# Optimization experiments

Hardware: AMD Instinct MI355X
Metric: run time of the kernel (lower is better)

## Reference

```python
import jax, jax.numpy as jnp
import numpy as np

B, N, E, D = 4, 4096, 2048, 128
MAX_L = 10


def setup_inputs() -> dict:
    key = jax.random.key(0)
    ks = jax.random.split(key, 8)
    x = jax.random.normal(ks[0], (B, N, D), dtype=jnp.float32)
    incidence = jax.random.uniform(ks[1], (B, N, E), dtype=jnp.float32)
    edge_orders = jax.random.randint(ks[2], (B, E), 0, MAX_L + 1)
    # positive normalizer to avoid division blow-up
    prefix_normalizer = jax.random.uniform(ks[3], (B, E), dtype=jnp.float32) + 0.5
    node_mask = jnp.ones((B, N), dtype=bool)
    edge_mask = jnp.ones((B, E), dtype=bool)
    n_nodes = jnp.full((B,), float(N), dtype=jnp.float32)
    # learned tables: Positional2DWeight(2, max_l+1, D, D) and PositionalWeight(max_l+1, 1, D)
    w_table = jax.random.normal(ks[4], (2, MAX_L + 1, D, D), dtype=jnp.float32) * (1.0 / np.sqrt(D))
    b_table = jax.random.normal(ks[5], (MAX_L + 1, D), dtype=jnp.float32) * 0.02
    return {"x": x, "incidence": incidence, "edge_orders": edge_orders,
            "prefix_normalizer": prefix_normalizer, "node_mask": node_mask,
            "edge_mask": edge_mask, "n_nodes": n_nodes,
            "w_table": w_table, "b_table": b_table}


def reference(x, incidence, edge_orders, prefix_normalizer, node_mask, edge_mask,
              n_nodes, w_table, b_table):
    # mask invalid nodes
    x = jnp.where(node_mask[..., None], x, 0.0)  # [B,N,D]
    # per-edge weight gather (the duplicated [B,E,D,D] tensors)
    w0 = w_table[0][edge_orders]  # [B,E,D,D]
    w1 = w_table[1][edge_orders]  # [B,E,D,D]
    w0_1 = w_table[0, 1]          # [D,D]
    w1_1 = w_table[1, 1]          # [D,D]
    # global mean pooling over nodes
    x0 = jnp.sum(x, axis=1, keepdims=True) / n_nodes[:, None, None]  # [B,1,D]
    # incidence-based V2E aggregation
    x1_e = jnp.einsum('bne,bnd->bed', incidence, x) / prefix_normalizer[..., None]
    x1_e = jnp.where(edge_mask[..., None], x1_e, 0.0)  # [B,E,D]
    # node branch: shared order-1 weights
    x_v = jnp.einsum('bnd,do->bno', x0, w0_1) + jnp.einsum('bnd,do->bno', x, w1_1)
    # edge branch: per-edge-order weights
    x_e = jnp.einsum('bd,bedo->beo', x0[:, 0], w0) + jnp.einsum('bed,bedo->beo', x1_e, w1)
    x_v = jnp.where(node_mask[..., None], x_v, 0.0)
    x_e = jnp.where(edge_mask[..., None], x_e, 0.0)
    # BiasE
    bias_e = b_table[edge_orders]            # [B,E,D]
    bias_1 = b_table[1][None, None, :]       # [1,1,D]
    x_v = jnp.where(node_mask[..., None], x_v + bias_1, 0.0)
    x_e = jnp.where(edge_mask[..., None], x_e + bias_e, 0.0)
    return x_v, x_e
```

## Files before the change

kernel.cpp:

```cpp
#include <hip/hip_runtime.h>

#define Bb 4
#define Nn 4096
#define Ee 2048
#define Dd 128
#define NL 11
#define TE 32
#define NCH 64

typedef unsigned short u16;
typedef unsigned int u32;
typedef __attribute__((ext_vector_type(8))) short short8;
typedef __attribute__((ext_vector_type(4))) float floatx4;

__device__ __forceinline__ u16 f2bf(float f) {
    union { float f; u32 i; } v; v.f = f;
    u32 r = v.i + 0x7fffu + ((v.i >> 16) & 1u);
    return (u16)(r >> 16);
}
__device__ __forceinline__ u32 pack2(float lo, float hi) {
    return (u32)f2bf(lo) | ((u32)f2bf(hi) << 16);
}

__global__ __launch_bounds__(128) void k_pool(const float* __restrict__ x,
                                              float* __restrict__ ws) {
    int b = blockIdx.x, ch = blockIdx.y, d = threadIdx.x;
    const float* p = x + ((size_t)b * Nn + (size_t)ch * 64) * Dd + d;
    float s = 0.f;
    for (int i = 0; i < 64; i++) s += p[(size_t)i * Dd];
    atomicAdd(&ws[b * Dd + d], s);
}

__global__ __launch_bounds__(128) void k_xe0(const float* __restrict__ ws,
                                             const float* __restrict__ wt,
                                             float* __restrict__ xe0) {
    int b = blockIdx.x, l = blockIdx.y, o = threadIdx.x;
    const float* w0 = wt + (size_t)l * Dd * Dd + o;
    float acc = 0.f;
    for (int d = 0; d < Dd; ++d)
        acc += ws[b * Dd + d] * w0[(size_t)d * Dd];
    xe0[(b * NL + l) * Dd + o] = acc * (1.0f / Nn);
}

__global__ __launch_bounds__(256) void k_trx(const float* __restrict__ x,
                                             u32* __restrict__ xt) {
    int b = blockIdx.x, n0 = blockIdx.y * 32, d0 = blockIdx.z * 32;
    int t = threadIdx.x;
    __shared__ float tile[32][33];
    int r = t >> 5, c = t & 31;
#pragma unroll
    for (int i = 0; i < 4; i++)
        tile[r + 8 * i][c] = x[((size_t)b * Nn + n0 + r + 8 * i) * Dd + d0 + c];
    __syncthreads();
#pragma unroll
    for (int i = 0; i < 2; i++) {
        int idx = t + 256 * i;
        int dl = idx >> 4, cp = idx & 15;
        u32 v = pack2(tile[2 * cp][dl], tile[2 * cp + 1][dl]);
        xt[(size_t)(b * Dd + d0 + dl) * (Nn / 2) + (n0 >> 1) + cp] = v;
    }
}

__global__ __launch_bounds__(256) void k_xv(const float* __restrict__ x,
                                            const float* __restrict__ wt,
                                            const float* __restrict__ bt,
                                            const float* __restrict__ xe0,
                                            float* __restrict__ outv) {
    int b = blockIdx.x, n0 = blockIdx.y * 32, t = threadIdx.x;
    __shared__ float xls[32][129];
    const float4* xs = (const float4*)(x + ((size_t)b * Nn + n0) * Dd);
#pragma unroll
    for (int i = 0; i < 4; i++) {
        int idx = t + 256 * i;
        int r = idx >> 5, c4 = idx & 31;
        float4 v = xs[idx];
        xls[r][c4 * 4 + 0] = v.x; xls[r][c4 * 4 + 1] = v.y;
        xls[r][c4 * 4 + 2] = v.z; xls[r][c4 * 4 + 3] = v.w;
    }
    __syncthreads();
    int o = t & 127, h = t >> 7;
    float base = xe0[(b * NL + 1) * Dd + o] + bt[Dd + o];
    float acc[16];
#pragma unroll
    for (int r = 0; r < 16; r++) acc[r] = base;
    const float* w11 = wt + (size_t)(NL + 1) * Dd * Dd + o;
    for (int d = 0; d < Dd; d++) {
        float wv = w11[(size_t)d * Dd];
#pragma unroll
        for (int r = 0; r < 16; r++) acc[r] += xls[h * 16 + r][d] * wv;
    }
    float* op = outv + ((size_t)b * Nn + n0 + h * 16) * Dd + o;
#pragma unroll
    for (int r = 0; r < 16; r++) op[(size_t)r * Dd] = acc[r];
}

__global__ __launch_bounds__(512) void k_edge(const float* __restrict__ inc,
                                              const u32* __restrict__ xt,
                                              const int* __restrict__ ord,
                                              const float* __restrict__ pref,
                                              const float* __restrict__ wt,
                                              const float* __restrict__ bt,
                                              const float* __restrict__ xe0,
                                              float* __restrict__ oute) {
    int b = blockIdx.x, et0 = blockIdx.y * TE;
    int t = threadIdx.x;
    __shared__ u32 incT[TE][36];
    __shared__ float x1s[TE][Dd + 1];
    __shared__ int ls[TE];
    __shared__ float pv[TE];
    if (t < TE) {
        ls[t] = ord[b * Ee + et0 + t];
        pv[t] = pref[b * Ee + et0 + t];
    }

    int lane = t & 63, w = t >> 6;
    int lm = lane & 15, quad = lane >> 4;
    int etile = w & 1, dt0 = (w >> 1) * 2;
    int eA = etile * 16 + lm;
    floatx4 acc0 = {0.f, 0.f, 0.f, 0.f}, acc1 = {0.f, 0.f, 0.f, 0.f};

    const u32* bb0 = xt + (size_t)(b * Dd + dt0 * 16 + lm) * (Nn / 2) + quad * 4;
    const u32* bb1 = xt + (size_t)(b * Dd + (dt0 + 1) * 16 + lm) * (Nn / 2) + quad * 4;
    int sn = t >> 3, sc4 = t & 7;

    for (int n0 = 0; n0 < Nn; n0 += NCH) {
        int ko = n0 >> 1;
        short8 b00 = *(const short8*)(bb0 + ko);
        short8 b10 = *(const short8*)(bb1 + ko);
        short8 b01 = *(const short8*)(bb0 + ko + 16);
        short8 b11 = *(const short8*)(bb1 + ko + 16);
        if (t < 256) {
            const float4* ra =
                (const float4*)(inc + ((size_t)b * Nn + n0 + 2 * sn) * Ee + et0);
            float4 va = ra[sc4];
            float4 vb = ra[sc4 + Ee / 4];
            incT[sc4 * 4 + 0][sn] = pack2(va.x, vb.x);
            incT[sc4 * 4 + 1][sn] = pack2(va.y, vb.y);
            incT[sc4 * 4 + 2][sn] = pack2(va.z, vb.z);
            incT[sc4 * 4 + 3][sn] = pack2(va.w, vb.w);
        }
        __syncthreads();
        short8 a0 = *(const short8*)&incT[eA][quad * 4];
        acc0 = __builtin_amdgcn_mfma_f32_16x16x32_bf16(a0, b00, acc0, 0, 0, 0);
        acc1 = __builtin_amdgcn_mfma_f32_16x16x32_bf16(a0, b10, acc1, 0, 0, 0);
        short8 a1 = *(const short8*)&incT[eA][16 + quad * 4];
        acc0 = __builtin_amdgcn_mfma_f32_16x16x32_bf16(a1, b01, acc0, 0, 0, 0);
        acc1 = __builtin_amdgcn_mfma_f32_16x16x32_bf16(a1, b11, acc1, 0, 0, 0);
        __syncthreads();
    }

#pragma unroll
    for (int r = 0; r < 4; r++) {
        int e = etile * 16 + quad * 4 + r;
        float rp = 1.0f / pv[e];
        x1s[e][dt0 * 16 + lm] = acc0[r] * rp;
        x1s[e][(dt0 + 1) * 16 + lm] = acc1[r] * rp;
    }
    __syncthreads();

    int o = t & 127, h = t >> 7;
    const float* w1base = wt + (size_t)NL * Dd * Dd;
    for (int j = 0; j < 8; j++) {
        int e = h * 8 + j;
        int l = ls[e];
        const float* w1 = w1base + (size_t)l * Dd * Dd + o;
        float a = xe0[(b * NL + l) * Dd + o] + bt[l * Dd + o];
#pragma unroll 4
        for (int d = 0; d < Dd; d++) a += x1s[e][d] * w1[(size_t)d * Dd];
        oute[((size_t)b * Ee + et0 + e) * Dd + o] = a;
    }
}

extern "C" void kernel_launch(void* const* d_in, const int* in_sizes, int n_in,
                              void* d_out, int out_size, void* d_ws,
                              size_t ws_size, hipStream_t stream) {
    const float* x    = (const float*)d_in[0];
    const float* inc  = (const float*)d_in[1];
    const int*   ord  = (const int*)d_in[2];
    const float* pref = (const float*)d_in[3];
    const float* wt   = (const float*)d_in[7];
    const float* bt   = (const float*)d_in[8];

    float* outv = (float*)d_out;
    float* oute = outv + (size_t)Bb * Nn * Dd;

    float* ws  = (float*)d_ws;
    float* xe0 = ws + 512;
    u32*   xt  = (u32*)(ws + 8192);

    hipMemsetAsync(d_ws, 0, 512 * sizeof(float), stream);
    k_pool<<<dim3(Bb, 64), 128, 0, stream>>>(x, ws);
    k_xe0<<<dim3(Bb, NL), 128, 0, stream>>>(ws, wt, xe0);
    k_trx<<<dim3(Bb, Nn / 32, Dd / 32), 256, 0, stream>>>(x, xt);
    k_xv<<<dim3(Bb, Nn / 32), 256, 0, stream>>>(x, wt, bt, xe0, outv);
    k_edge<<<dim3(Bb, Ee / TE), 512, 0, stream>>>(inc, xt, ord, pref, wt, bt,
                                                  xe0, oute);
}
```

Baseline: 335.9 us.

## Split edge kernel into pipelined MFMA einsum and order-bucketed MFMA epilogue

The fused edge kernel is replaced by three parts. A double-buffered, register-prefetched bf16 MFMA kernel computes the incidence-x aggregation into a bf16 intermediate. Edges are then bucketed by order with count, prefix and scatter kernels, so a grouped MFMA epilogue can apply each order's weight matrix from LDS. The node branch also moves from scalar FP32 FMAs to bf16 MFMA. This removes the per-edge scalar matvec and the globally re-read weights, at the cost of extra launches, atomics and more bf16 rounding of weights and activations.

```diff
diff --git a/kernel.cpp b/kernel.cpp
--- a/kernel.cpp
+++ b/kernel.cpp
@@ -5,8 +5,6 @@
 #define Ee 2048
 #define Dd 128
 #define NL 11
-#define TE 32
-#define NCH 64
 
 typedef unsigned short u16;
 typedef unsigned int u32;
@@ -19,26 +17,29 @@
     return (u16)(r >> 16);
 }
 __device__ __forceinline__ u32 pack2(float lo, float hi) {
-    return (u32)f2bf(lo) | ((u32)f2bf(hi) << 16);
-}
+    union { float f; u32 i; } a, b; a.f = lo; b.f = hi;
+    u32 x = a.i + 0x7fffu + ((a.i >> 16) & 1u);
+    u32 y = b.i + 0x7fffu + ((b.i >> 16) & 1u);
+    return (x >> 16) | (y & 0xffff0000u);
+}
+union S8U { u32 u[4]; short8 s; };
 
 __global__ __launch_bounds__(128) void k_pool(const float* __restrict__ x,
-                                              float* __restrict__ ws) {
+                                              float* __restrict__ sums) {
     int b = blockIdx.x, ch = blockIdx.y, d = threadIdx.x;
     const float* p = x + ((size_t)b * Nn + (size_t)ch * 64) * Dd + d;
     float s = 0.f;
     for (int i = 0; i < 64; i++) s += p[(size_t)i * Dd];
-    atomicAdd(&ws[b * Dd + d], s);
-}
-
-__global__ __launch_bounds__(128) void k_xe0(const float* __restrict__ ws,
+    atomicAdd(&sums[b * Dd + d], s);
+}
+
+__global__ __launch_bounds__(128) void k_xe0(const float* __restrict__ sums,
                                              const float* __restrict__ wt,
                                              float* __restrict__ xe0) {
     int b = blockIdx.x, l = blockIdx.y, o = threadIdx.x;
     const float* w0 = wt + (size_t)l * Dd * Dd + o;
     float acc = 0.f;
-    for (int d = 0; d < Dd; ++d)
-        acc += ws[b * Dd + d] * w0[(size_t)d * Dd];
+    for (int d = 0; d < Dd; ++d) acc += sums[b * Dd + d] * w0[(size_t)d * Dd];
     xe0[(b * NL + l) * Dd + o] = acc * (1.0f / Nn);
 }
 
@@ -54,10 +55,109 @@
     __syncthreads();
 #pragma unroll
     for (int i = 0; i < 2; i++) {
-        int idx = t + 256 * i;
-        int dl = idx >> 4, cp = idx & 15;
+        int idx2 = t + 256 * i;
+        int dl = idx2 >> 4, cp = idx2 & 15;
         u32 v = pack2(tile[2 * cp][dl], tile[2 * cp + 1][dl]);
         xt[(size_t)(b * Dd + d0 + dl) * (Nn / 2) + (n0 >> 1) + cp] = v;
+    }
+}
+
+__global__ __launch_bounds__(256) void k_count(const int* __restrict__ ord,
+                                               int* __restrict__ cnt) {
+    int gid = blockIdx.x * 256 + threadIdx.x;
+    int b = gid >> 11, e = gid & 2047;
+    atomicAdd(&cnt[b * NL + ord[b * Ee + e]], 1);
+}
+__global__ __launch_bounds__(64) void k_prefix(const int* __restrict__ cnt,
+                                               int* __restrict__ offs,
+                                               int* __restrict__ idx) {
+    int t = threadIdx.x;
+    if (t == 0) {
+        int off = 0;
+        for (int i = 0; i < Bb * NL; i++) {
+            offs[i] = off;
+            off += (cnt[i] + 15) & ~15;
+        }
+    }
+    for (int i = t; i < 8960; i += 64) idx[i] = 0;
+}
+__global__ __launch_bounds__(256) void k_scatter(const int* __restrict__ ord,
+                                                 const int* __restrict__ offs,
+                                                 int* __restrict__ cur,
+                                                 int* __restrict__ idx) {
+    int gid = blockIdx.x * 256 + threadIdx.x;
+    int b = gid >> 11, e = gid & 2047;
+    int bk = b * NL + ord[b * Ee + e];
+    int pos = offs[bk] + atomicAdd(&cur[bk], 1);
+    idx[pos] = e;
+}
+
+__global__ __launch_bounds__(256, 2) void k_einsum(const float* __restrict__ inc,
+                                                   const u32* __restrict__ xt,
+                                                   const float* __restrict__ pref,
+                                                   u16* __restrict__ x1e) {
+    int b = blockIdx.x, et0 = blockIdx.y * 16, t = threadIdx.x;
+    __shared__ u32 bufA[2][16][68];
+    int ur = t >> 2, uc = t & 3;
+    const float* src0 = inc + (size_t)b * Nn * Ee + et0 + 4 * uc;
+
+    int w = t >> 6, lane = t & 63, lm = lane & 15, quad = lane >> 4;
+    const u32* bp0 = xt + ((size_t)b * Dd + 32 * w + lm) * (Nn / 2);
+    const u32* bp1 = bp0 + (size_t)16 * (Nn / 2);
+    floatx4 acc0 = {0.f, 0.f, 0.f, 0.f}, acc1 = {0.f, 0.f, 0.f, 0.f};
+
+    float4 pa0, pb0, pa1, pb1;
+    {
+        const float* p = src0 + (size_t)(2 * ur) * Ee;
+        pa0 = *(const float4*)p; pb0 = *(const float4*)(p + Ee);
+        p = src0 + (size_t)(128 + 2 * ur) * Ee;
+        pa1 = *(const float4*)p; pb1 = *(const float4*)(p + Ee);
+    }
+    bufA[0][4 * uc + 0][ur] = pack2(pa0.x, pb0.x);
+    bufA[0][4 * uc + 1][ur] = pack2(pa0.y, pb0.y);
+    bufA[0][4 * uc + 2][ur] = pack2(pa0.z, pb0.z);
+    bufA[0][4 * uc + 3][ur] = pack2(pa0.w, pb0.w);
+    __syncthreads();
+
+    for (int i = 0; i < 32; i++) {
+        int nxt = (i + 2 < 32) ? i + 2 : 31;
+        const float* p = src0 + (size_t)(128 * nxt + 2 * ur) * Ee;
+        if ((i & 1) == 0) { pa0 = *(const float4*)p; pb0 = *(const float4*)(p + Ee); }
+        else             { pa1 = *(const float4*)p; pb1 = *(const float4*)(p + Ee); }
+
+        int cb = i & 1;
+        u32 ko = (u32)(64 * i) + quad * 4;
+#pragma unroll
+        for (int ks = 0; ks < 4; ks++) {
+            short8 A = *(const short8*)&bufA[cb][lm][ks * 16 + quad * 4];
+            short8 B0 = *(const short8*)(bp0 + ko + ks * 16);
+            short8 B1 = *(const short8*)(bp1 + ko + ks * 16);
+            acc0 = __builtin_amdgcn_mfma_f32_16x16x32_bf16(A, B0, acc0, 0, 0, 0);
+            acc1 = __builtin_amdgcn_mfma_f32_16x16x32_bf16(A, B1, acc1, 0, 0, 0);
+        }
+        if (i < 31) {
+            int nb = 1 - cb;
+            if ((i & 1) == 0) {
+                bufA[nb][4 * uc + 0][ur] = pack2(pa1.x, pb1.x);
+                bufA[nb][4 * uc + 1][ur] = pack2(pa1.y, pb1.y);
+                bufA[nb][4 * uc + 2][ur] = pack2(pa1.z, pb1.z);
+                bufA[nb][4 * uc + 3][ur] = pack2(pa1.w, pb1.w);
+            } else {
+                bufA[nb][4 * uc + 0][ur] = pack2(pa0.x, pb0.x);
+                bufA[nb][4 * uc + 1][ur] = pack2(pa0.y, pb0.y);
+                bufA[nb][4 * uc + 2][ur] = pack2(pa0.z, pb0.z);
+                bufA[nb][4 * uc + 3][ur] = pack2(pa0.w, pb0.w);
+            }
+        }
+        __syncthreads();
+    }
+#pragma unroll
+    for (int r = 0; r < 4; r++) {
+        int e = et0 + quad * 4 + r;
+        float rp = 1.0f / pref[b * Ee + e];
+        u16* q = x1e + ((size_t)b * Ee + e) * Dd;
+        q[32 * w + lm] = f2bf(acc0[r] * rp);
+        q[32 * w + 16 + lm] = f2bf(acc1[r] * rp);
     }
 }
 
@@ -66,108 +166,111 @@
                                             const float* __restrict__ bt,
                                             const float* __restrict__ xe0,
                                             float* __restrict__ outv) {
-    int b = blockIdx.x, n0 = blockIdx.y * 32, t = threadIdx.x;
-    __shared__ float xls[32][129];
-    const float4* xs = (const float4*)(x + ((size_t)b * Nn + n0) * Dd);
-#pragma unroll
-    for (int i = 0; i < 4; i++) {
-        int idx = t + 256 * i;
-        int r = idx >> 5, c4 = idx & 31;
-        float4 v = xs[idx];
-        xls[r][c4 * 4 + 0] = v.x; xls[r][c4 * 4 + 1] = v.y;
-        xls[r][c4 * 4 + 2] = v.z; xls[r][c4 * 4 + 3] = v.w;
+    int b = blockIdx.x, n0 = blockIdx.y * 64, t = threadIdx.x;
+    __shared__ u16 wT16[128][136];
+    __shared__ float baseLds[128];
+    const float* w11 = wt + (size_t)(NL + 1) * Dd * Dd;
+    {
+        int o4 = (t & 31) * 4, dr = t >> 5;
+#pragma unroll
+        for (int p = 0; p < 16; p++) {
+            int d = dr + p * 8;
+            float4 v = *(const float4*)&w11[(size_t)d * Dd + o4];
+            wT16[o4 + 0][d] = f2bf(v.x);
+            wT16[o4 + 1][d] = f2bf(v.y);
+            wT16[o4 + 2][d] = f2bf(v.z);
+            wT16[o4 + 3][d] = f2bf(v.w);
+        }
+        if (t < 128) baseLds[t] = xe0[(b * NL + 1) * Dd + t] + bt[Dd + t];
     }
     __syncthreads();
-    int o = t & 127, h = t >> 7;
-    float base = xe0[(b * NL + 1) * Dd + o] + bt[Dd + o];
-    float acc[16];
-#pragma unroll
-    for (int r = 0; r < 16; r++) acc[r] = base;
-    const float* w11 = wt + (size_t)(NL + 1) * Dd * Dd + o;
-    for (int d = 0; d < Dd; d++) {
-        float wv = w11[(size_t)d * Dd];
-#pragma unroll
-        for (int r = 0; r < 16; r++) acc[r] += xls[h * 16 + r][d] * wv;
-    }
-    float* op = outv + ((size_t)b * Nn + n0 + h * 16) * Dd + o;
-#pragma unroll
-    for (int r = 0; r < 16; r++) op[(size_t)r * Dd] = acc[r];
-}
-
-__global__ __launch_bounds__(512) void k_edge(const float* __restrict__ inc,
-                                              const u32* __restrict__ xt,
-                                              const int* __restrict__ ord,
-                                              const float* __restrict__ pref,
-                                              const float* __restrict__ wt,
-                                              const float* __restrict__ bt,
-                                              const float* __restrict__ xe0,
-                                              float* __restrict__ oute) {
-    int b = blockIdx.x, et0 = blockIdx.y * TE;
-    int t = threadIdx.x;
-    __shared__ u32 incT[TE][36];
-    __shared__ float x1s[TE][Dd + 1];
-    __shared__ int ls[TE];
-    __shared__ float pv[TE];
-    if (t < TE) {
-        ls[t] = ord[b * Ee + et0 + t];
-        pv[t] = pref[b * Ee + et0 + t];
-    }
-
-    int lane = t & 63, w = t >> 6;
-    int lm = lane & 15, quad = lane >> 4;
-    int etile = w & 1, dt0 = (w >> 1) * 2;
-    int eA = etile * 16 + lm;
-    floatx4 acc0 = {0.f, 0.f, 0.f, 0.f}, acc1 = {0.f, 0.f, 0.f, 0.f};
-
-    const u32* bb0 = xt + (size_t)(b * Dd + dt0 * 16 + lm) * (Nn / 2) + quad * 4;
-    const u32* bb1 = xt + (size_t)(b * Dd + (dt0 + 1) * 16 + lm) * (Nn / 2) + quad * 4;
-    int sn = t >> 3, sc4 = t & 7;
-
-    for (int n0 = 0; n0 < Nn; n0 += NCH) {
-        int ko = n0 >> 1;
-        short8 b00 = *(const short8*)(bb0 + ko);
-        short8 b10 = *(const short8*)(bb1 + ko);
-        short8 b01 = *(const short8*)(bb0 + ko + 16);
-        short8 b11 = *(const short8*)(bb1 + ko + 16);
-        if (t < 256) {
-            const float4* ra =
-                (const float4*)(inc + ((size_t)b * Nn + n0 + 2 * sn) * Ee + et0);
-            float4 va = ra[sc4];
-            float4 vb = ra[sc4 + Ee / 4];
-            incT[sc4 * 4 + 0][sn] = pack2(va.x, vb.x);
-            incT[sc4 * 4 + 1][sn] = pack2(va.y, vb.y);
-            incT[sc4 * 4 + 2][sn] = pack2(va.z, vb.z);
-            incT[sc4 * 4 + 3][sn] = pack2(va.w, vb.w);
-        }
-        __syncthreads();
-        short8 a0 = *(const short8*)&incT[eA][quad * 4];
-        acc0 = __builtin_amdgcn_mfma_f32_16x16x32_bf16(a0, b00, acc0, 0, 0, 0);
-        acc1 = __builtin_amdgcn_mfma_f32_16x16x32_bf16(a0, b10, acc1, 0, 0, 0);
-        short8 a1 = *(const short8*)&incT[eA][16 + quad * 4];
-        acc0 = __builtin_amdgcn_mfma_f32_16x16x32_bf16(a1, b01, acc0, 0, 0, 0);
-        acc1 = __builtin_amdgcn_mfma_f32_16x16x32_bf16(a1, b11, acc1, 0, 0, 0);
-        __syncthreads();
-    }
-
-#pragma unroll
-    for (int r = 0; r < 4; r++) {
-        int e = etile * 16 + quad * 4 + r;
-        float rp = 1.0f / pv[e];
-        x1s[e][dt0 * 16 + lm] = acc0[r] * rp;
-        x1s[e][(dt0 + 1) * 16 + lm] = acc1[r] * rp;
+
+    int w = t >> 6, lane = t & 63, lm = lane & 15, quad = lane >> 4;
+    const float* xrow = x + ((size_t)b * Nn + n0 + w * 16 + lm) * Dd;
+    floatx4 acc[8];
+#pragma unroll
+    for (int ot = 0; ot < 8; ot++) acc[ot] = (floatx4){0.f, 0.f, 0.f, 0.f};
+#pragma unroll
+    for (int ks = 0; ks < 4; ks++) {
+        float4 va = *(const float4*)(xrow + ks * 32 + quad * 8);
+        float4 vb = *(const float4*)(xrow + ks * 32 + quad * 8 + 4);
+        S8U A;
+        A.u[0] = pack2(va.x, va.y); A.u[1] = pack2(va.z, va.w);
+        A.u[2] = pack2(vb.x, vb.y); A.u[3] = pack2(vb.z, vb.w);
+#pragma unroll
+        for (int ot = 0; ot < 8; ot++) {
+            short8 Bf = *(const short8*)&wT16[ot * 16 + lm][ks * 32 + quad * 8];
+            acc[ot] = __builtin_amdgcn_mfma_f32_16x16x32_bf16(A.s, Bf, acc[ot], 0, 0, 0);
+        }
+    }
+#pragma unroll
+    for (int ot = 0; ot < 8; ot++) {
+        float basev = baseLds[ot * 16 + lm];
+#pragma unroll
+        for (int r = 0; r < 4; r++)
+            outv[((size_t)b * Nn + n0 + w * 16 + quad * 4 + r) * Dd + ot * 16 + lm] =
+                acc[ot][r] + basev;
+    }
+}
+
+__global__ __launch_bounds__(256) void k_epi(const u16* __restrict__ x1e,
+                                             const float* __restrict__ wt,
+                                             const float* __restrict__ bt,
+                                             const float* __restrict__ xe0,
+                                             const int* __restrict__ cnt,
+                                             const int* __restrict__ offs,
+                                             const int* __restrict__ idx,
+                                             float* __restrict__ oute) {
+    int blk = blockIdx.x, bb = blk / NL, l = blk % NL, t = threadIdx.x;
+    int cntv = cnt[blk], off = offs[blk];
+    __shared__ u16 wT16[128][136];
+    __shared__ float baseLds[128];
+    const float* w1 = wt + (size_t)(NL + l) * Dd * Dd;
+    {
+        int o4 = (t & 31) * 4, dr = t >> 5;
+#pragma unroll
+        for (int p = 0; p < 16; p++) {
+            int d = dr + p * 8;
+            float4 v = *(const float4*)&w1[(size_t)d * Dd + o4];
+            wT16[o4 + 0][d] = f2bf(v.x);
+            wT16[o4 + 1][d] = f2bf(v.y);
+            wT16[o4 + 2][d] = f2bf(v.z);
+            wT16[o4 + 3][d] = f2bf(v.w);
+        }
+        if (t < 128) baseLds[t] = xe0[(bb * NL + l) * Dd + t] + bt[l * Dd + t];
     }
     __syncthreads();
 
-    int o = t & 127, h = t >> 7;
-    const float* w1base = wt + (size_t)NL * Dd * Dd;
-    for (int j = 0; j < 8; j++) {
-        int e = h * 8 + j;
-        int l = ls[e];
-        const float* w1 = w1base + (size_t)l * Dd * Dd + o;
-        float a = xe0[(b * NL + l) * Dd + o] + bt[l * Dd + o];
-#pragma unroll 4
-        for (int d = 0; d < Dd; d++) a += x1s[e][d] * w1[(size_t)d * Dd];
-        oute[((size_t)b * Ee + et0 + e) * Dd + o] = a;
+    int w = t >> 6, lane = t & 63, lm = lane & 15, quad = lane >> 4;
+    int ntile = (cntv + 15) >> 4;
+    for (int j = w; j < ntile; j += 4) {
+        int rA = idx[off + j * 16 + lm];
+        int4 rid = *(const int4*)&idx[off + j * 16 + quad * 4];
+        const u16* ap = x1e + ((size_t)bb * Ee + rA) * Dd;
+        floatx4 acc[8];
+#pragma unroll
+        for (int ot = 0; ot < 8; ot++) acc[ot] = (floatx4){0.f, 0.f, 0.f, 0.f};
+#pragma unroll
+        for (int ks = 0; ks < 4; ks++) {
+            short8 A = *(const short8*)(ap + ks * 32 + quad * 8);
+#pragma unroll
+            for (int ot = 0; ot < 8; ot++) {
+                short8 Bf = *(const short8*)&wT16[ot * 16 + lm][ks * 32 + quad * 8];
+                acc[ot] = __builtin_amdgcn_mfma_f32_16x16x32_bf16(A, Bf, acc[ot], 0, 0, 0);
+            }
+        }
+        int rowbase = j * 16 + quad * 4;
+#pragma unroll
+        for (int ot = 0; ot < 8; ot++) {
+            float basev = baseLds[ot * 16 + lm];
+#pragma unroll
+            for (int r = 0; r < 4; r++) {
+                if (rowbase + r < cntv) {
+                    int e = ((const int*)&rid)[r];
+                    oute[((size_t)bb * Ee + e) * Dd + ot * 16 + lm] = acc[ot][r] + basev;
+                }
+            }
+        }
     }
 }
 
@@ -184,15 +287,24 @@
     float* outv = (float*)d_out;
     float* oute = outv + (size_t)Bb * Nn * Dd;
 
-    float* ws  = (float*)d_ws;
-    float* xe0 = ws + 512;
-    u32*   xt  = (u32*)(ws + 8192);
-
-    hipMemsetAsync(d_ws, 0, 512 * sizeof(float), stream);
-    k_pool<<<dim3(Bb, 64), 128, 0, stream>>>(x, ws);
-    k_xe0<<<dim3(Bb, NL), 128, 0, stream>>>(ws, wt, xe0);
+    float* ws   = (float*)d_ws;
+    float* sums = ws;
+    float* xe0  = ws + 512;
+    int*   cnt  = (int*)(ws + 6144);
+    int*   offs = (int*)(ws + 6192);
+    int*   cur  = (int*)(ws + 6240);
+    u32*   xt   = (u32*)(ws + 8192);
+    int*   idx  = (int*)(ws + 8192 + 1048576);
+    u16*   x1e  = (u16*)(ws + 8192 + 1048576 + 8960);
+
+    hipMemsetAsync(d_ws, 0, 6288 * sizeof(float), stream);
+    k_pool<<<dim3(Bb, 64), 128, 0, stream>>>(x, sums);
+    k_xe0<<<dim3(Bb, NL), 128, 0, stream>>>(sums, wt, xe0);
     k_trx<<<dim3(Bb, Nn / 32, Dd / 32), 256, 0, stream>>>(x, xt);
-    k_xv<<<dim3(Bb, Nn / 32), 256, 0, stream>>>(x, wt, bt, xe0, outv);
-    k_edge<<<dim3(Bb, Ee / TE), 512, 0, stream>>>(inc, xt, ord, pref, wt, bt,
-                                                  xe0, oute);
-}
+    k_count<<<32, 256, 0, stream>>>(ord, cnt);
+    k_prefix<<<1, 64, 0, stream>>>(cnt, offs, idx);
+    k_scatter<<<32, 256, 0, stream>>>(ord, offs, cur, idx);
+    k_einsum<<<dim3(Bb, Ee / 16), 256, 0, stream>>>(inc, xt, pref, x1e);
+    k_xv<<<dim3(Bb, Nn / 64), 256, 0, stream>>>(x, wt, bt, xe0, outv);
+    k_epi<<<Bb * NL, 256, 0, stream>>>(x1e, wt, bt, xe0, cnt, offs, idx, oute);
+}
```

Measured after the change: 346.0 us. +3.0%, slower.
